# Kernel tuning notes

Measured on AMD Instinct MI355X. Metric: run time of the kernel, lower is better.

Reference implementation:

```python
import jax, jax.numpy as jnp
import numpy as np

ENC_UNITS = 50
FEAT = 4
T = 100
B = 256


def param_activation(x, min_val, max_val):
    # tanh(x) * scale + min_val + scale, scale = (max-min)/2  -> range (min_val, max_val)
    scale = (max_val - min_val) / 2.0
    return jnp.tanh(x) * scale + min_val + scale


def lstm(x, kernel, rec_kernel, bias):
    # Keras LSTM, gate order i,f,c,o; returns final hidden state h_T. x: [B,T,F]
    u = ENC_UNITS
    # precompute input projections for all timesteps: [B,T,4u]
    zx = jnp.einsum('btf,fg->btg', x, kernel) + bias

    def step(carry, z_t):
        h, c = carry
        z = z_t + h @ rec_kernel  # [B,4u]
        i = jax.nn.sigmoid(z[:, :u])
        f = jax.nn.sigmoid(z[:, u:2 * u])
        g = jnp.tanh(z[:, 2 * u:3 * u])
        o = jax.nn.sigmoid(z[:, 3 * u:])
        c = f * c + i * g
        h = o * jnp.tanh(c)
        return (h, c), None

    h0 = jnp.zeros((x.shape[0], u), x.dtype)
    (h, c), _ = jax.lax.scan(step, (h0, h0), jnp.swapaxes(zx, 0, 1))
    return h


def setup_inputs() -> dict:
    key = jax.random.key(0)
    ks = jax.random.split(key, 16)
    x_scaled = jax.random.normal(ks[0], (B, T, FEAT), dtype=jnp.float32)
    # state: keep vel/dv/dx in a physically sane positive range; dx (channel 3) away from 0
    state = jax.random.uniform(ks[1], (B, T, FEAT), dtype=jnp.float32, minval=1.0, maxval=30.0)
    g = 1.0 / np.sqrt(ENC_UNITS)
    params = {
        'lstm_kernel': jax.random.normal(ks[2], (FEAT, 4 * ENC_UNITS), jnp.float32) * 0.1,
        'lstm_rec_kernel': jax.random.normal(ks[3], (ENC_UNITS, 4 * ENC_UNITS), jnp.float32) * g,
        'lstm_bias': jnp.zeros((4 * ENC_UNITS,), jnp.float32),
        'w_desired_v': jax.random.normal(ks[4], (ENC_UNITS, 1), jnp.float32) * g,
        'b_desired_v': jnp.zeros((1,), jnp.float32),
        'w_desired_tgap': jax.random.normal(ks[5], (ENC_UNITS, 1), jnp.float32) * g,
        'b_desired_tgap': jnp.zeros((1,), jnp.float32),
        'w_min_jamx': jax.random.normal(ks[6], (ENC_UNITS, 1), jnp.float32) * g,
        'b_min_jamx': jnp.ones((1,), jnp.float32),  # keep min_jamx mostly > 0 past relu
        'w_max_act': jax.random.normal(ks[7], (ENC_UNITS, 1), jnp.float32) * g,
        'b_max_act': jnp.zeros((1,), jnp.float32),
        'w_min_act': jax.random.normal(ks[8], (ENC_UNITS, 1), jnp.float32) * g,
        'b_min_act': jnp.zeros((1,), jnp.float32),
    }
    return {'x_scaled': x_scaled, 'state': state, **params}


def reference(x_scaled, state, lstm_kernel, lstm_rec_kernel, lstm_bias,
              w_desired_v, b_desired_v, w_desired_tgap, b_desired_tgap,
              w_min_jamx, b_min_jamx, w_max_act, b_max_act, w_min_act, b_min_act):
    h_t = lstm(x_scaled, lstm_kernel, lstm_rec_kernel, lstm_bias)  # [B, 50]

    desired_v = param_activation(h_t @ w_desired_v + b_desired_v, 15.0, 35.0)     # [B,1]
    desired_tgap = param_activation(h_t @ w_desired_tgap + b_desired_tgap, 0.5, 3.0)
    min_jamx = jax.nn.relu(h_t @ w_min_jamx + b_min_jamx)
    max_act = param_activation(h_t @ w_max_act + b_max_act, 0.5, 3.0)
    min_act = param_activation(h_t @ w_min_act + b_min_act, 0.5, 4.0)
    idm_param = jnp.concatenate([desired_v, desired_tgap, min_jamx, max_act, min_act], axis=1)  # [B,5]

    # Vectorized IDM over all 100 timesteps at once (steps are data-independent).
    vel = state[:, :, 0]  # [B,T]
    dv = state[:, :, 2]
    dx = state[:, :, 3]
    two_sqrt_ab = 2.0 * jnp.sqrt(max_act * min_act)  # [B,1]
    desired_gap = min_jamx + desired_tgap * vel + (vel * dv) / two_sqrt_ab  # [B,T]
    act = max_act * (1.0 - ((vel / desired_v) ** 4.0 + (desired_gap / dx) ** 2.0))  # [B,T]
    act_seq = act[:, :, None]  # [B,T,1]
    return act_seq, idm_param
```

## Files before the change

kernel.cpp:

```cpp
#include <hip/hip_runtime.h>
#include <hip/hip_fp16.h>
#include <math.h>
#include <stdint.h>

#define U 50
#define TT 100
#define BB 256

typedef _Float16 half2v __attribute__((ext_vector_type(2)));

__device__ __forceinline__ float dot2_acc(uint32_t h2, uint32_t w2, float c) {
#if __has_builtin(__builtin_amdgcn_fdot2)
    return __builtin_amdgcn_fdot2(__builtin_bit_cast(half2v, h2),
                                  __builtin_bit_cast(half2v, w2), c, false);
#else
    half2v a = __builtin_bit_cast(half2v, h2);
    half2v b = __builtin_bit_cast(half2v, w2);
    return fmaf((float)a.x, (float)b.x, fmaf((float)a.y, (float)b.y, c));
#endif
}

__device__ __forceinline__ float sigmoid_fast(float x) {
    return 1.0f / (1.0f + __expf(-x));
}
__device__ __forceinline__ float tanh_fast(float x) {
    float e = __expf(2.0f * x);
    return 1.0f - 2.0f / (e + 1.0f);
}
__device__ __forceinline__ float param_act(float x, float mn, float mx) {
    float scale = 0.5f * (mx - mn);
    return tanh_fast(x) * scale + mn + scale;
}

#define BAR() do {                                            \
    asm volatile("s_waitcnt lgkmcnt(0)" ::: "memory");        \
    __builtin_amdgcn_s_barrier();                             \
    asm volatile("" ::: "memory");                            \
} while (0)

__global__ __launch_bounds__(256, 1) void encoder_kernel(
    const float* __restrict__ x,
    const float* __restrict__ state,
    const float* __restrict__ kernel,
    const float* __restrict__ rec,
    const float* __restrict__ bias,
    const float* __restrict__ w_dv, const float* __restrict__ b_dv,
    const float* __restrict__ w_dt, const float* __restrict__ b_dt,
    const float* __restrict__ w_mj, const float* __restrict__ b_mj,
    const float* __restrict__ w_ma, const float* __restrict__ b_ma,
    const float* __restrict__ w_mi, const float* __restrict__ b_mi,
    float* __restrict__ out)
{
    const int b   = blockIdx.x;
    const int tid = threadIdx.x;
    const int w   = tid >> 6;
    const int l   = tid & 63;
    const int cl  = (l < U) ? l : (U - 1);

    __shared__ __align__(16) float4 xlds[TT];
    __shared__ __align__(16) _Float16 h16[64];
    __shared__ float zex[2][4][64];
    __shared__ float idm[8];

    uint32_t wpk[25];
    #pragma unroll
    for (int j = 0; j < 25; ++j) {
        float r0 = rec[(2 * j) * 200 + w * U + cl];
        float r1 = rec[(2 * j + 1) * 200 + w * U + cl];
        half2v p; p.x = (_Float16)r0; p.y = (_Float16)r1;
        wpk[j] = __builtin_bit_cast(uint32_t, p);
    }
    #pragma unroll
    for (int j = 0; j < 25; ++j) asm volatile("" : "+v"(wpk[j]));

    float kc[4];
    #pragma unroll
    for (int f = 0; f < 4; ++f) kc[f] = kernel[f * 200 + w * U + cl];
    float bz = bias[w * U + cl];

    const float4* __restrict__ xg = (const float4*)(x + (size_t)b * TT * 4);
    if (tid < TT) xlds[tid] = xg[tid];
    if (tid < 64) h16[tid] = (_Float16)0.0f;
    __syncthreads();

    float cstate = 0.0f;
    uint32_t hvu[25];
    #pragma unroll
    for (int j = 0; j < 25; ++j) hvu[j] = 0u;

    const uint4* __restrict__ hq = (const uint4*)h16;
    const uint32_t* __restrict__ hd = (const uint32_t*)h16;

    for (int t = 0; t < TT; ++t) {
        float4 x4 = xlds[t];

        float z = fmaf(x4.x, kc[0], fmaf(x4.y, kc[1],
                  fmaf(x4.z, kc[2], fmaf(x4.w, kc[3], bz))));
        float a0 = 0.f, a1 = 0.f;
        #pragma unroll
        for (int j = 0; j < 24; j += 2) {
            a0 = dot2_acc(hvu[j], wpk[j], a0);
            a1 = dot2_acc(hvu[j + 1], wpk[j + 1], a1);
        }
        a0 = dot2_acc(hvu[24], wpk[24], a0);
        z += a0 + a1;

        float nl = (w == 2) ? tanh_fast(z) : sigmoid_fast(z);
        zex[t & 1][w][l] = nl;

        BAR();

        const int buf = t & 1;
        float gi = zex[buf][0][l];
        float gf = zex[buf][1][l];
        float gg = zex[buf][2][l];
        float go = zex[buf][3][l];
        cstate = fmaf(gf, cstate, gi * gg);
        float hn = go * tanh_fast(cstate);
        if (l < U) h16[l] = (_Float16)hn;

        #pragma unroll
        for (int q = 0; q < 6; ++q) {
            uint4 v = hq[q];
            hvu[4 * q + 0] = v.x; hvu[4 * q + 1] = v.y;
            hvu[4 * q + 2] = v.z; hvu[4 * q + 3] = v.w;
        }
        hvu[24] = hd[24];
    }

    if (tid < 5) {
        const float* wv = (tid == 0) ? w_dv : (tid == 1) ? w_dt :
                          (tid == 2) ? w_mj : (tid == 3) ? w_ma : w_mi;
        const float* bv = (tid == 0) ? b_dv : (tid == 1) ? b_dt :
                          (tid == 2) ? b_mj : (tid == 3) ? b_ma : b_mi;
        float s = bv[0];
        #pragma unroll
        for (int j = 0; j < U; ++j) s = fmaf((float)h16[j], wv[j], s);
        float v;
        if (tid == 0)      v = param_act(s, 15.0f, 35.0f);
        else if (tid == 1) v = param_act(s, 0.5f, 3.0f);
        else if (tid == 2) v = fmaxf(s, 0.0f);
        else if (tid == 3) v = param_act(s, 0.5f, 3.0f);
        else               v = param_act(s, 0.5f, 4.0f);
        idm[tid] = v;
        out[BB * TT + b * 5 + tid] = v;
    }
    __syncthreads();

    const float desired_v    = idm[0];
    const float desired_tgap = idm[1];
    const float min_jamx     = idm[2];
    const float max_act      = idm[3];
    const float min_act      = idm[4];
    const float inv_tsab = 1.0f / (2.0f * sqrtf(max_act * min_act));
    const float inv_dv   = 1.0f / desired_v;

    const float4* __restrict__ sb4 = (const float4*)(state + (size_t)b * TT * 4);
    for (int t = tid; t < TT; t += 256) {
        float4 s4 = sb4[t];
        float vel = s4.x;
        float dv  = s4.z;
        float dx  = s4.w;
        float dgap = fmaf(desired_tgap, vel, fmaf(vel * dv, inv_tsab, min_jamx));
        float r1 = vel * inv_dv;
        r1 = r1 * r1;
        r1 = r1 * r1;
        float r2 = dgap / dx;
        r2 = r2 * r2;
        out[b * TT + t] = max_act * (1.0f - (r1 + r2));
    }
}

extern "C" void kernel_launch(void* const* d_in, const int* in_sizes, int n_in,
                              void* d_out, int out_size, void* d_ws, size_t ws_size,
                              hipStream_t stream) {
    const float* x      = (const float*)d_in[0];
    const float* state  = (const float*)d_in[1];
    const float* kern   = (const float*)d_in[2];
    const float* rec    = (const float*)d_in[3];
    const float* bias   = (const float*)d_in[4];
    const float* w_dv   = (const float*)d_in[5];
    const float* b_dv   = (const float*)d_in[6];
    const float* w_dt   = (const float*)d_in[7];
    const float* b_dt   = (const float*)d_in[8];
    const float* w_mj   = (const float*)d_in[9];
    const float* b_mj   = (const float*)d_in[10];
    const float* w_ma   = (const float*)d_in[11];
    const float* b_ma   = (const float*)d_in[12];
    const float* w_mi   = (const float*)d_in[13];
    const float* b_mi   = (const float*)d_in[14];
    float* out = (float*)d_out;

    encoder_kernel<<<BB, 256, 0, stream>>>(
        x, state, kern, rec, bias,
        w_dv, b_dv, w_dt, b_dt, w_mj, b_mj, w_ma, b_ma, w_mi, b_mi,
        out);
}
```

Before: 44.87 us.

## Compute LSTM recurrent step with MFMA and fold input projection into K

Replaces the per-thread fp16 dot2 recurrent matvec with 16x16x32 MFMA instructions, padding the K dimension to 64. The input projection (4 features) and the bias are folded into the K dimension by appending x_t and a constant 1 to the shared hidden vector. This removes the per-lane 25-register hidden reload and the separate input FMA chain. In exchange, most MFMA output is wasted since the batch dimension is 1 per block, and x and bias now pass through fp16, which costs some precision.

```diff
diff --git a/kernel.cpp b/kernel.cpp
--- a/kernel.cpp
+++ b/kernel.cpp
@@ -7,18 +7,8 @@
 #define TT 100
 #define BB 256
 
-typedef _Float16 half2v __attribute__((ext_vector_type(2)));
-
-__device__ __forceinline__ float dot2_acc(uint32_t h2, uint32_t w2, float c) {
-#if __has_builtin(__builtin_amdgcn_fdot2)
-    return __builtin_amdgcn_fdot2(__builtin_bit_cast(half2v, h2),
-                                  __builtin_bit_cast(half2v, w2), c, false);
-#else
-    half2v a = __builtin_bit_cast(half2v, h2);
-    half2v b = __builtin_bit_cast(half2v, w2);
-    return fmaf((float)a.x, (float)b.x, fmaf((float)a.y, (float)b.y, c));
-#endif
-}
+typedef _Float16 f16x8 __attribute__((ext_vector_type(8)));
+typedef float    f32x4 __attribute__((ext_vector_type(4)));
 
 __device__ __forceinline__ float sigmoid_fast(float x) {
     return 1.0f / (1.0f + __expf(-x));
@@ -55,77 +45,86 @@
     const int tid = threadIdx.x;
     const int w   = tid >> 6;
     const int l   = tid & 63;
-    const int cl  = (l < U) ? l : (U - 1);
+    const int c   = l & 15;
+    const int q   = l >> 4;
 
     __shared__ __align__(16) float4 xlds[TT];
-    __shared__ __align__(16) _Float16 h16[64];
+    __shared__ __align__(16) _Float16 hbb[64];
     __shared__ float zex[2][4][64];
     __shared__ float idm[8];
 
-    uint32_t wpk[25];
+    f16x8 wf[4][2];
     #pragma unroll
-    for (int j = 0; j < 25; ++j) {
-        float r0 = rec[(2 * j) * 200 + w * U + cl];
-        float r1 = rec[(2 * j + 1) * 200 + w * U + cl];
-        half2v p; p.x = (_Float16)r0; p.y = (_Float16)r1;
-        wpk[j] = __builtin_bit_cast(uint32_t, p);
+    for (int nt = 0; nt < 4; ++nt) {
+        const int uu = 16 * nt + c;
+        #pragma unroll
+        for (int ks = 0; ks < 2; ++ks) {
+            f16x8 f;
+            #pragma unroll
+            for (int e = 0; e < 8; ++e) {
+                const int j = 32 * ks + 8 * q + e;
+                float v = 0.0f;
+                if (uu < U) {
+                    if (j < U)           v = rec[j * 200 + w * U + uu];
+                    else if (j < U + 4)  v = kernel[(j - U) * 200 + w * U + uu];
+                    else if (j == U + 4) v = bias[w * U + uu];
+                }
+                f[e] = (_Float16)v;
+            }
+            wf[nt][ks] = f;
+        }
     }
-    #pragma unroll
-    for (int j = 0; j < 25; ++j) asm volatile("" : "+v"(wpk[j]));
 
-    float kc[4];
-    #pragma unroll
-    for (int f = 0; f < 4; ++f) kc[f] = kernel[f * 200 + w * U + cl];
-    float bz = bias[w * U + cl];
-
-    const float4* __restrict__ xg = (const float4*)(x + (size_t)b * TT * 4);
-    if (tid < TT) xlds[tid] = xg[tid];
-    if (tid < 64) h16[tid] = (_Float16)0.0f;
+    if (tid < TT) xlds[tid] = ((const float4*)(x + (size_t)b * TT * 4))[tid];
+    if (tid < 64) {
+        _Float16 v = (_Float16)0.0f;
+        if (tid >= U && tid < U + 4) v = (_Float16)x[(size_t)b * TT * 4 + (tid - U)];
+        if (tid == U + 4) v = (_Float16)1.0f;
+        hbb[tid] = v;
+    }
     __syncthreads();
 
     float cstate = 0.0f;
-    uint32_t hvu[25];
-    #pragma unroll
-    for (int j = 0; j < 25; ++j) hvu[j] = 0u;
-
-    const uint4* __restrict__ hq = (const uint4*)h16;
-    const uint32_t* __restrict__ hd = (const uint32_t*)h16;
+    const uint4* __restrict__ hq = (const uint4*)hbb;
+    const float* __restrict__ xf = (const float*)xlds;
+    const f32x4 zero4 = {0.f, 0.f, 0.f, 0.f};
 
     for (int t = 0; t < TT; ++t) {
-        float4 x4 = xlds[t];
+        const int buf = t & 1;
 
-        float z = fmaf(x4.x, kc[0], fmaf(x4.y, kc[1],
-                  fmaf(x4.z, kc[2], fmaf(x4.w, kc[3], bz))));
-        float a0 = 0.f, a1 = 0.f;
-        #pragma unroll
-        for (int j = 0; j < 24; j += 2) {
-            a0 = dot2_acc(hvu[j], wpk[j], a0);
-            a1 = dot2_acc(hvu[j + 1], wpk[j + 1], a1);
-        }
-        a0 = dot2_acc(hvu[24], wpk[24], a0);
-        z += a0 + a1;
+        uint4 a0u = hq[q];
+        uint4 a1u = hq[4 + q];
+        f16x8 A0 = __builtin_bit_cast(f16x8, a0u);
+        f16x8 A1 = __builtin_bit_cast(f16x8, a1u);
+
+        float xnext = 0.0f;
+        if (l >= U && l < U + 4)
+            xnext = xf[((t + 1 < TT) ? (t + 1) : t) * 4 + (l - U)];
+
+        f32x4 a0 = __builtin_amdgcn_mfma_f32_16x16x32_f16(A0, wf[0][0], zero4, 0, 0, 0);
+        f32x4 a1 = __builtin_amdgcn_mfma_f32_16x16x32_f16(A0, wf[1][0], zero4, 0, 0, 0);
+        f32x4 a2 = __builtin_amdgcn_mfma_f32_16x16x32_f16(A0, wf[2][0], zero4, 0, 0, 0);
+        f32x4 a3 = __builtin_amdgcn_mfma_f32_16x16x32_f16(A0, wf[3][0], zero4, 0, 0, 0);
+        a0 = __builtin_amdgcn_mfma_f32_16x16x32_f16(A1, wf[0][1], a0, 0, 0, 0);
+        a1 = __builtin_amdgcn_mfma_f32_16x16x32_f16(A1, wf[1][1], a1, 0, 0, 0);
+        a2 = __builtin_amdgcn_mfma_f32_16x16x32_f16(A1, wf[2][1], a2, 0, 0, 0);
+        a3 = __builtin_amdgcn_mfma_f32_16x16x32_f16(A1, wf[3][1], a3, 0, 0, 0);
+
+        float z = (q == 0) ? a0[0] : (q == 1) ? a1[0] : (q == 2) ? a2[0] : a3[0];
 
         float nl = (w == 2) ? tanh_fast(z) : sigmoid_fast(z);
-        zex[t & 1][w][l] = nl;
+        zex[buf][w][l] = nl;
 
         BAR();
 
-        const int buf = t & 1;
         float gi = zex[buf][0][l];
         float gf = zex[buf][1][l];
         float gg = zex[buf][2][l];
         float go = zex[buf][3][l];
         cstate = fmaf(gf, cstate, gi * gg);
         float hn = go * tanh_fast(cstate);
-        if (l < U) h16[l] = (_Float16)hn;
-
-        #pragma unroll
-        for (int q = 0; q < 6; ++q) {
-            uint4 v = hq[q];
-            hvu[4 * q + 0] = v.x; hvu[4 * q + 1] = v.y;
-            hvu[4 * q + 2] = v.z; hvu[4 * q + 3] = v.w;
-        }
-        hvu[24] = hd[24];
+        if (l < U)              hbb[l] = (_Float16)hn;
+        else if (l < U + 4)     hbb[l] = (_Float16)xnext;
     }
 
     if (tid < 5) {
@@ -135,7 +134,7 @@
                           (tid == 2) ? b_mj : (tid == 3) ? b_ma : b_mi;
         float s = bv[0];
         #pragma unroll
-        for (int j = 0; j < U; ++j) s = fmaf((float)h16[j], wv[j], s);
+        for (int j = 0; j < U; ++j) s = fmaf((float)hbb[j], wv[j], s);
         float v;
         if (tid == 0)      v = param_act(s, 15.0f, 35.0f);
         else if (tid == 1) v = param_act(s, 0.5f, 3.0f);
@@ -147,27 +146,22 @@
     }
     __syncthreads();
 
-    const float desired_v    = idm[0];
-    const float desired_tgap = idm[1];
-    const float min_jamx     = idm[2];
-    const float max_act      = idm[3];
-    const float min_act      = idm[4];
-    const float inv_tsab = 1.0f / (2.0f * sqrtf(max_act * min_act));
-    const float inv_dv   = 1.0f / desired_v;
-
-    const float4* __restrict__ sb4 = (const float4*)(state + (size_t)b * TT * 4);
-    for (int t = tid; t < TT; t += 256) {
-        float4 s4 = sb4[t];
-        float vel = s4.x;
-        float dv  = s4.z;
-        float dx  = s4.w;
+    if (tid < TT) {
+        const float desired_v    = idm[0];
+        const float desired_tgap = idm[1];
+        const float min_jamx     = idm[2];
+        const float max_act      = idm[3];
+        const float min_act      = idm[4];
+        const float inv_tsab = 1.0f / (2.0f * sqrtf(max_act * min_act));
+        const float inv_dv   = 1.0f / desired_v;
+        float4 s4 = ((const float4*)(state + (size_t)b * TT * 4))[tid];
+        float vel = s4.x, dv = s4.z, dx = s4.w;
         float dgap = fmaf(desired_tgap, vel, fmaf(vel * dv, inv_tsab, min_jamx));
         float r1 = vel * inv_dv;
-        r1 = r1 * r1;
-        r1 = r1 * r1;
+        r1 = r1 * r1; r1 = r1 * r1;
         float r2 = dgap / dx;
         r2 = r2 * r2;
-        out[b * TT + t] = max_act * (1.0f - (r1 + r2));
+        out[b * TT + tid] = max_act * (1.0f - (r1 + r2));
     }
 }
 
```

Measured after the change: 51.04 us. 13.8% more time.
